# Kernel optimization log

Measured on AMD Instinct MI355X. Metric: run time of the kernel, lower is better.

The kernel has to match this reference:

```python
import jax, jax.numpy as jnp
import numpy as np

K = 7          # involution kernel size
PAD = 3        # (K-1)//2
G = 4          # groups = out_channels // group_channels
GC = 16        # group_channels
EPS = 1e-5     # BatchNorm eps


def _bn(x, g, b, m, v):
    # eval-mode BatchNorm2d over channel dim of NCHW
    scale = g / jnp.sqrt(v + EPS)
    return x * scale[:, None, None] + (b - m * scale)[:, None, None]


def _conv1x1(x, w, b=None):
    y = jnp.einsum('bchw,oc->bohw', x, w)
    if b is not None:
        y = y + b[:, None, None]
    return y


def _gelu(x):
    return jax.nn.gelu(x, approximate=False)  # torch nn.GELU default (erf)


def _involution(x, wr, gr, br, mr, vr, ws, bs):
    # kernel-generation branch: 1x1 reduce -> BN -> ReLU -> 1x1 span
    r = jax.nn.relu(_bn(_conv1x1(x, wr), gr, br, mr, vr))
    w = _conv1x1(r, ws, bs)                       # [B, G*K*K, H, W]
    B, _, H, W = w.shape
    w = w.reshape(B, G, K * K, H, W)
    # unfold x into KxK patches (channel-major then row-major kernel pos, matching nn.Unfold)
    xp = jnp.pad(x, ((0, 0), (0, 0), (PAD, PAD), (PAD, PAD)))
    patches = jnp.stack([xp[:, :, i:i + H, j:j + W]
                         for i in range(K) for j in range(K)], axis=2)  # [B, C, KK, H, W]
    patches = patches.reshape(B, G, GC, K * K, H, W)
    out = jnp.einsum('bgkhw,bgckhw->bgchw', w, patches)  # per-pixel dynamic kernel apply
    return out.reshape(B, G * GC, H, W)


def setup_inputs() -> dict:
    key = jax.random.key(0)
    ks = jax.random.split(key, 24)
    B, Cin, Cout, H, W = 4, 32, 64, 128, 128
    red = Cout // 4
    n = lambda k, s, sc: jax.random.normal(k, s, jnp.float32) * sc
    u = lambda k, s: jax.random.uniform(k, s, jnp.float32, 0.5, 1.5)
    inp = {
        'x': n(ks[0], (B, Cin, H, W), 1.0),
        'w1': n(ks[1], (Cout, Cin), 0.15),
        # involution: reduce conv + BN, span conv
        'wr': n(ks[2], (red, Cout), 0.12), 'gr': u(ks[3], (red,)), 'br': n(ks[4], (red,), 0.05),
        'mr': n(ks[5], (red,), 0.05), 'vr': u(ks[6], (red,)),
        'ws': n(ks[7], (K * K * G, red), 0.1), 'bs': n(ks[8], (K * K * G,), 0.02),
        # BN after involution
        'g1': u(ks[9], (Cout,)), 'b1': n(ks[10], (Cout,), 0.05),
        'm1': n(ks[11], (Cout,), 0.05), 'v1': u(ks[12], (Cout,)),
        # convblock2
        'w2': n(ks[13], (Cout, Cout), 0.12),
        'g2': u(ks[14], (Cout,)), 'b2': n(ks[15], (Cout,), 0.05),
        'm2': n(ks[16], (Cout,), 0.05), 'v2': u(ks[17], (Cout,)),
        # mapping (residual projection) conv has bias=True by default
        'wm': n(ks[18], (Cout, Cin), 0.15), 'bmap': n(ks[19], (Cout,), 0.02),
        'gm': u(ks[20], (Cout,)), 'betam': n(ks[21], (Cout,), 0.05),
        'mm': n(ks[22], (Cout,), 0.05), 'vm': u(ks[23], (Cout,)),
    }
    return inp


def reference(x, w1, wr, gr, br, mr, vr, ws, bs, g1, b1, m1, v1,
              w2, g2, b2, m2, v2, wm, bmap, gm, betam, mm, vm):
    x1 = _gelu(_conv1x1(x, w1))                                  # convblock
    x1 = _gelu(_bn(_involution(x1, wr, gr, br, mr, vr, ws, bs),
                   g1, b1, m1, v1))                              # involution + BN + GELU
    x1 = _bn(_conv1x1(x1, w2), g2, b2, m2, v2)                   # convblock2
    skip = _bn(_conv1x1(x, wm, bmap), gm, betam, mm, vm)         # mapping (Cin != Cout)
    return _gelu(x1 + skip)
```

## Files before the change

### kernel.cpp

```cpp
#include <hip/hip_runtime.h>
#include <hip/hip_bf16.h>
#include <math.h>

#define HW    16384
#define Bsz   4
#define CIN   32
#define COUT  64
#define RED   16
#define KKN   49
#define GG    4
#define PW    134
#define NHALO 25152
#define NZB   99
#define NPXB  1024

typedef __hip_bfloat16 bf16;
typedef __attribute__((ext_vector_type(8))) short bf16x8;
typedef __attribute__((ext_vector_type(4))) float f32x4;

__device__ __forceinline__ float gelu_f(float x) {
    return 0.5f * x * (1.0f + erff(x * 0.70710678118654752f));
}
__device__ __forceinline__ void unpack_bf2(unsigned u, float& lo, float& hi) {
    lo = __uint_as_float(u << 16);
    hi = __uint_as_float(u & 0xffff0000u);
}
__device__ __forceinline__ unsigned pack_bf2(float lo, float hi) {
    unsigned a = __float_as_uint(lo), b = __float_as_uint(hi);
    a += 0x7fff + ((a >> 16) & 1);
    b += 0x7fff + ((b >> 16) & 1);
    return (a >> 16) | (b & 0xffff0000u);
}
__device__ __forceinline__ unsigned short bf16r(float v) {
    unsigned a = __float_as_uint(v);
    a += 0x7fff + ((a >> 16) & 1);
    return (unsigned short)(a >> 16);
}

#define OFF_RBUF  9437184
#define OFF_PAR   22020096
#define OFF_XBF   22085632
#define PSHC_F 16
#define PSMV_F 80
#define PSC1_F 144
#define PSH1_F 208
#define BCAT 12288

__global__ __launch_bounds__(256, 4) void k1_all(
    const float* __restrict__ x, const float* __restrict__ w1,
    const float* __restrict__ wr, const float* __restrict__ gr,
    const float* __restrict__ br, const float* __restrict__ mr,
    const float* __restrict__ vr,
    const float* __restrict__ g1, const float* __restrict__ b1,
    const float* __restrict__ m1, const float* __restrict__ v1,
    const float* __restrict__ w2, const float* __restrict__ g2,
    const float* __restrict__ b2, const float* __restrict__ m2,
    const float* __restrict__ v2,
    const float* __restrict__ wm, const float* __restrict__ bmap,
    const float* __restrict__ gm, const float* __restrict__ betam,
    const float* __restrict__ mm, const float* __restrict__ vm,
    char* __restrict__ parb, unsigned* __restrict__ x1pad,
    unsigned short* __restrict__ xbf, float* __restrict__ rbuf)
{
    __shared__ float x1f[4][16][65];
    int bid = blockIdx.x, t = threadIdx.x;

    if (bid >= NPXB) {
        int hb = bid - NPXB;
        if (hb < NZB) {
            unsigned i = (unsigned)hb * 256u + (unsigned)t;
            if (i < NHALO) {
                unsigned plane = i / 1572u;
                unsigned rem = i - plane * 1572u;
                unsigned row, col;
                if (rem < 804u) {
                    unsigned rr = rem / 134u;
                    col = rem - rr * 134u;
                    row = rr < 3u ? rr : rr + 128u;
                } else {
                    unsigned r2 = rem - 804u;
                    unsigned rr = r2 / 6u;
                    unsigned cc = r2 - rr * 6u;
                    row = rr + 3u;
                    col = cc < 3u ? cc : cc + 128u;
                }
                uint4* q = (uint4*)x1pad + ((size_t)(plane * PW + row) * PW + col) * 2;
                q[0] = make_uint4(0u, 0u, 0u, 0u);
                q[1] = make_uint4(0u, 0u, 0u, 0u);
            }
        } else {
            float* parf = (float*)parb;
            unsigned short* wcat = (unsigned short*)(parb + BCAT);
            for (int i = t; i < 64 * 96; i += 256) {
                int o = i / 96, c = i - o * 96;
                float v;
                if (c < 64) {
                    float s2 = g2[o] * rsqrtf(v2[o] + 1e-5f);
                    float sm = gm[o] * rsqrtf(vm[o] + 1e-5f);
                    v = w2[o * COUT + c] * (s2 / sm);
                } else {
                    v = wm[o * CIN + (c - 64)];
                }
                wcat[i] = bf16r(v);
            }
            if (t < 64) {
                float s2 = g2[t] * rsqrtf(v2[t] + 1e-5f);
                float sm = gm[t] * rsqrtf(vm[t] + 1e-5f);
                parf[PSHC_F + t] = (b2[t] - m2[t] * s2) + (betam[t] + (bmap[t] - mm[t]) * sm);
                parf[PSMV_F + t] = sm;
                float s1 = g1[t] * rsqrtf(v1[t] + 1e-5f);
                parf[PSC1_F + t] = s1;
                parf[PSH1_F + t] = b1[t] - m1[t] * s1;
            }
        }
        return;
    }

    int lane = t & 63;
    int wave = t >> 6;
    int m15 = lane & 15, quad = lane >> 4;
    int base_gpx = bid * 64 + wave * 16;
    int b   = base_gpx >> 14;
    int px0 = base_gpx & (HW - 1);

    int gpx = base_gpx + m15;
    int p   = gpx & (HW - 1);
    unsigned apk[4];
#pragma unroll
    for (int d = 0; d < 4; ++d) {
        float lo = x[((size_t)(b * CIN + quad * 8 + 2 * d)) * HW + p];
        float hi = x[((size_t)(b * CIN + quad * 8 + 2 * d + 1)) * HW + p];
        apk[d] = pack_bf2(lo, hi);
    }
    union BU { uint4 q; bf16x8 v; };
    BU au; au.q = make_uint4(apk[0], apk[1], apk[2], apk[3]);
    bf16x8 Af = au.v;
    *(uint4*)&xbf[(size_t)gpx * 32 + quad * 8] = au.q;

    f32x4 acc[4];
#pragma unroll
    for (int nt = 0; nt < 4; ++nt) {
        int o = nt * 16 + m15;
        unsigned bpk[4];
#pragma unroll
        for (int d = 0; d < 4; ++d) {
            float lo = w1[o * CIN + quad * 8 + 2 * d];
            float hi = w1[o * CIN + quad * 8 + 2 * d + 1];
            bpk[d] = pack_bf2(lo, hi);
        }
        BU bu; bu.q = make_uint4(bpk[0], bpk[1], bpk[2], bpk[3]);
        f32x4 z = {0.f, 0.f, 0.f, 0.f};
        acc[nt] = __builtin_amdgcn_mfma_f32_16x16x32_bf16(Af, bu.v, z, 0, 0, 0);
    }
#pragma unroll
    for (int nt = 0; nt < 4; ++nt)
#pragma unroll
        for (int reg = 0; reg < 4; ++reg)
            x1f[wave][quad * 4 + reg][nt * 16 + m15] = gelu_f(acc[nt][reg]);

    __syncthreads();

    {
        int pxl = lane >> 2, g = lane & 3;
        int pp = px0 + pxl, h = pp >> 7, w = pp & 127;
        unsigned pk[8];
#pragma unroll
        for (int d = 0; d < 8; ++d)
            pk[d] = pack_bf2(x1f[wave][pxl][g * 16 + 2 * d],
                             x1f[wave][pxl][g * 16 + 2 * d + 1]);
        unsigned* xo = x1pad +
            ((size_t)((b * GG + g) * PW + (h + 3)) * PW + (w + 3)) * 8;
        *(uint4*)xo       = make_uint4(pk[0], pk[1], pk[2], pk[3]);
        *(uint4*)(xo + 4) = make_uint4(pk[4], pk[5], pk[6], pk[7]);
    }

    float sc  = gr[m15] * rsqrtf(vr[m15] + 1e-5f);
    float rsh = br[m15] - mr[m15] * sc;
    f32x4 racc = {0.f, 0.f, 0.f, 0.f};
#pragma unroll
    for (int kt = 0; kt < 2; ++kt) {
        bf16x8 A2, B2;
#pragma unroll
        for (int j = 0; j < 8; ++j) {
            A2[j] = (short)bf16r(x1f[wave][m15][kt * 32 + quad * 8 + j]);
            B2[j] = (short)bf16r(wr[m15 * 64 + kt * 32 + quad * 8 + j] * sc);
        }
        racc = __builtin_amdgcn_mfma_f32_16x16x32_bf16(A2, B2, racc, 0, 0, 0);
    }
#pragma unroll
    for (int reg = 0; reg < 4; ++reg) {
        int gp = base_gpx + quad * 4 + reg;
        rbuf[(size_t)gp * 16 + m15] = fmaxf(racc[reg] + rsh, 0.f);
    }
}

#define TAPC(kk, TA, TB)                                                  \
    {                                                                     \
        const float* wk = wrow + (kk) * RED;                              \
        float s = brow[(kk)];                                             \
        s += rA.x * wk[0];  s += rA.y * wk[1];                            \
        s += rA.z * wk[2];  s += rA.w * wk[3];                            \
        s += rB.x * wk[4];  s += rB.y * wk[5];                            \
        s += rB.z * wk[6];  s += rB.w * wk[7];                            \
        s += rC.x * wk[8];  s += rC.y * wk[9];                            \
        s += rC.z * wk[10]; s += rC.w * wk[11];                           \
        s += rD.x * wk[12]; s += rD.y * wk[13];                           \
        s += rD.z * wk[14]; s += rD.w * wk[15];                           \
        float lo, hi;                                                     \
        unpack_bf2((TA).x, lo, hi); acc[0] += s*lo; acc[1] += s*hi;       \
        unpack_bf2((TA).y, lo, hi); acc[2] += s*lo; acc[3] += s*hi;       \
        unpack_bf2((TA).z, lo, hi); acc[4] += s*lo; acc[5] += s*hi;       \
        unpack_bf2((TA).w, lo, hi); acc[6] += s*lo; acc[7] += s*hi;       \
        unpack_bf2((TB).x, lo, hi); acc[8] += s*lo; acc[9] += s*hi;       \
        unpack_bf2((TB).y, lo, hi); acc[10]+= s*lo; acc[11]+= s*hi;       \
        unpack_bf2((TB).z, lo, hi); acc[12]+= s*lo; acc[13]+= s*hi;       \
        unpack_bf2((TB).w, lo, hi); acc[14]+= s*lo; acc[15]+= s*hi;       \
    }

__global__ __launch_bounds__(256, 4) void k34_fused(
    const unsigned* __restrict__ x1pad, const float* __restrict__ rbuf,
    const float* __restrict__ wsp, const float* __restrict__ bsp,
    const char* __restrict__ parb, const unsigned short* __restrict__ xbf,
    float* __restrict__ out)
{
    __shared__ unsigned short x2t[64][88];

    const float* par = (const float*)parb;
    int t = threadIdx.x;
    int b = blockIdx.x >> 8;
    int pxblk = (blockIdx.x & 255) << 6;

    {
        int pxl = t & 63;
        int g = __builtin_amdgcn_readfirstlane(t >> 6);
        int p = pxblk + pxl;
        int h = p >> 7, w0 = p & 127;
        int bg = b * GG + g;

        const float4* rp = (const float4*)&rbuf[((size_t)b * HW + p) * 16];
        float4 rA = rp[0], rB = rp[1], rC = rp[2], rD = rp[3];

        const float* wrow = wsp + g * KKN * RED;
        const float* brow = bsp + g * KKN;
        const unsigned* tp = x1pad + ((size_t)(bg * PW + h) * PW + w0) * 8;

        float acc[RED];
#pragma unroll
        for (int c = 0; c < RED; ++c) acc[c] = 0.f;

        const unsigned* pn = tp + 8;
        uint4 cA0 = *(const uint4*)tp, cB0 = *(const uint4*)(tp + 4);
        uint4 cA1 = *(const uint4*)pn, cB1 = *(const uint4*)(pn + 4);
        int jj = 1;
#pragma unroll 1
        for (int k = 0; k < KKN - 1; k += 2) {
            const unsigned* q0 = pn + (jj == 6 ? (PW - 6) * 8 : 8);
            int j0 = (jj == 6) ? 0 : jj + 1;
            const unsigned* q1 = q0 + (j0 == 6 ? (PW - 6) * 8 : 8);
            jj = (j0 == 6) ? 0 : j0 + 1;
            uint4 nA0 = *(const uint4*)q0, nB0 = *(const uint4*)(q0 + 4);
            uint4 nA1 = *(const uint4*)q1, nB1 = *(const uint4*)(q1 + 4);
            TAPC(k,     cA0, cB0);
            TAPC(k + 1, cA1, cB1);
            pn = q1;
            cA0 = nA0; cB0 = nB0; cA1 = nA1; cB1 = nB1;
        }
        TAPC(KKN - 1, cA0, cB0);

        unsigned pk[8];
#pragma unroll
        for (int d = 0; d < 8; ++d) {
            int ch0 = g * RED + 2 * d, ch1 = ch0 + 1;
            float v0 = gelu_f(par[PSC1_F + ch0] * acc[2 * d]     + par[PSH1_F + ch0]);
            float v1 = gelu_f(par[PSC1_F + ch1] * acc[2 * d + 1] + par[PSH1_F + ch1]);
            pk[d] = pack_bf2(v0, v1);
        }
        unsigned* xo = (unsigned*)&x2t[pxl][g * RED];
        *(uint4*)xo       = make_uint4(pk[0], pk[1], pk[2], pk[3]);
        *(uint4*)(xo + 4) = make_uint4(pk[4], pk[5], pk[6], pk[7]);
    }

    __syncthreads();

    {
        int lane = t & 63, wave = t >> 6;
        int m15  = lane & 15;
        int quad = lane >> 4;
        int pxl0 = wave * 16;
        int px0  = pxblk + pxl0;

        const unsigned short* wcat = (const unsigned short*)(parb + BCAT);

        bf16x8 Bf[3][4];
#pragma unroll
        for (int kt = 0; kt < 3; ++kt)
#pragma unroll
            for (int nt = 0; nt < 4; ++nt)
                Bf[kt][nt] = *(const bf16x8*)&wcat[(nt * 16 + m15) * 96 + kt * 32 + quad * 8];

        bf16x8 Af[3];
        Af[0] = *(const bf16x8*)&x2t[pxl0 + m15][quad * 8];
        Af[1] = *(const bf16x8*)&x2t[pxl0 + m15][32 + quad * 8];
        Af[2] = *(const bf16x8*)&xbf[((size_t)(b * HW + px0 + m15)) * 32 + quad * 8];

        f32x4 acc[4];
#pragma unroll
        for (int nt = 0; nt < 4; ++nt) acc[nt] = (f32x4){0.f, 0.f, 0.f, 0.f};
#pragma unroll
        for (int kt = 0; kt < 3; ++kt)
#pragma unroll
            for (int nt = 0; nt < 4; ++nt)
                acc[nt] = __builtin_amdgcn_mfma_f32_16x16x32_bf16(
                    Af[kt], Bf[kt][nt], acc[nt], 0, 0, 0);

#pragma unroll
        for (int nt = 0; nt < 4; ++nt) {
            int o = nt * 16 + m15;
            float smv = par[PSMV_F + o], sh = par[PSHC_F + o];
            float* op = out + (size_t)(b * COUT + o) * HW + px0 + quad * 4;
#pragma unroll
            for (int reg = 0; reg < 4; ++reg)
                op[reg] = gelu_f(smv * acc[nt][reg] + sh);
        }
    }
}

extern "C" void kernel_launch(void* const* d_in, const int* in_sizes, int n_in,
                              void* d_out, int out_size, void* d_ws, size_t ws_size,
                              hipStream_t stream) {
    const float* x    = (const float*)d_in[0];
    const float* w1   = (const float*)d_in[1];
    const float* wr   = (const float*)d_in[2];
    const float* gr   = (const float*)d_in[3];
    const float* br   = (const float*)d_in[4];
    const float* mr   = (const float*)d_in[5];
    const float* vr   = (const float*)d_in[6];
    const float* wsp  = (const float*)d_in[7];
    const float* bsp  = (const float*)d_in[8];
    const float* g1   = (const float*)d_in[9];
    const float* b1   = (const float*)d_in[10];
    const float* m1   = (const float*)d_in[11];
    const float* v1   = (const float*)d_in[12];
    const float* w2   = (const float*)d_in[13];
    const float* g2   = (const float*)d_in[14];
    const float* b2   = (const float*)d_in[15];
    const float* m2   = (const float*)d_in[16];
    const float* v2   = (const float*)d_in[17];
    const float* wm   = (const float*)d_in[18];
    const float* bmap = (const float*)d_in[19];
    const float* gm   = (const float*)d_in[20];
    const float* betam= (const float*)d_in[21];
    const float* mm   = (const float*)d_in[22];
    const float* vm   = (const float*)d_in[23];

    unsigned*       x1pad = (unsigned*)d_ws;
    float*          rbuf  = (float*)((char*)d_ws + OFF_RBUF);
    char*           parb  = (char*)d_ws + OFF_PAR;
    unsigned short* xbf   = (unsigned short*)((char*)d_ws + OFF_XBF);

    k1_all<<<NPXB + NZB + 1, 256, 0, stream>>>(
        x, w1, wr, gr, br, mr, vr, g1, b1, m1, v1,
        w2, g2, b2, m2, v2, wm, bmap, gm, betam, mm, vm,
        parb, x1pad, xbf, rbuf);
    k34_fused<<<Bsz * GG * HW / 256, 256, 0, stream>>>(
        x1pad, rbuf, wsp, bsp, parb, xbf, (float*)d_out);
}
```

Before: 153.3 us.

## Stage involution halo rows in double-buffered shared memory for tap reuse

The involution tap loop previously read all 49 neighbourhood taps per pixel directly from global memory, so each input pixel was fetched up to 49 times by neighbouring threads. The block now cooperatively loads one padded 70-pixel row per group into a double-buffered LDS row buffer, prefetches the next row from global while computing the current row's 7 taps out of LDS, and synchronises once per row. This cuts redundant global/L2 traffic at the cost of about 18 KB of extra LDS per block, which may lower occupancy, plus seven block barriers.

```diff
diff --git a/kernel.cpp b/kernel.cpp
--- a/kernel.cpp
+++ b/kernel.cpp
@@ -13,6 +13,7 @@
 #define NHALO 25152
 #define NZB   99
 #define NPXB  1024
+#define ROWCHK 560
 
 typedef __hip_bfloat16 bf16;
 typedef __attribute__((ext_vector_type(8))) short bf16x8;
@@ -194,6 +195,10 @@
     }
 }
 
+#define LDTAP(J)                                                          \
+    uint4 A##J = rb[aidx + (J)];                                          \
+    uint4 B##J = rb[aidx + 70 + (J)];
+
 #define TAPC(kk, TA, TB)                                                  \
     {                                                                     \
         const float* wk = wrow + (kk) * RED;                              \
@@ -223,49 +228,83 @@
     const char* __restrict__ parb, const unsigned short* __restrict__ xbf,
     float* __restrict__ out)
 {
+    __shared__ uint4 rowbuf[2][ROWCHK];
     __shared__ unsigned short x2t[64][88];
 
     const float* par = (const float*)parb;
     int t = threadIdx.x;
     int b = blockIdx.x >> 8;
     int pxblk = (blockIdx.x & 255) << 6;
+    int bh = pxblk >> 7, bw = pxblk & 127;
+    int b4 = b * GG;
+
+    int c0 = t, c1 = t + 256, c2 = t + 512;
+    int has2 = (c2 < ROWCHK);
+    int g0 = c0 / 140, r0c = c0 - g0 * 140;
+    int hf0 = r0c / 70, px0c = r0c - hf0 * 70;
+    int g1c = c1 / 140, r1c = c1 - g1c * 140;
+    int hf1 = r1c / 70, px1c = r1c - hf1 * 70;
+    int g2c = has2 ? c2 / 140 : 3;
+    int r2c = (has2 ? c2 : ROWCHK - 1) - g2c * 140;
+    int hf2 = r2c / 70, px2c = r2c - hf2 * 70;
+    size_t off0 = ((size_t)((b4 + g0) * PW + bh) * PW + (bw + px0c)) * 8 + hf0 * 4;
+    size_t off1 = ((size_t)((b4 + g1c) * PW + bh) * PW + (bw + px1c)) * 8 + hf1 * 4;
+    size_t off2 = ((size_t)((b4 + g2c) * PW + bh) * PW + (bw + px2c)) * 8 + hf2 * 4;
 
     {
         int pxl = t & 63;
         int g = __builtin_amdgcn_readfirstlane(t >> 6);
-        int p = pxblk + pxl;
-        int h = p >> 7, w0 = p & 127;
-        int bg = b * GG + g;
-
-        const float4* rp = (const float4*)&rbuf[((size_t)b * HW + p) * 16];
+        int aidx = g * 140 + pxl;
+
+        const float4* rp = (const float4*)&rbuf[((size_t)b * HW + pxblk + pxl) * 16];
         float4 rA = rp[0], rB = rp[1], rC = rp[2], rD = rp[3];
 
         const float* wrow = wsp + g * KKN * RED;
         const float* brow = bsp + g * KKN;
-        const unsigned* tp = x1pad + ((size_t)(bg * PW + h) * PW + w0) * 8;
 
         float acc[RED];
 #pragma unroll
         for (int c = 0; c < RED; ++c) acc[c] = 0.f;
 
-        const unsigned* pn = tp + 8;
-        uint4 cA0 = *(const uint4*)tp, cB0 = *(const uint4*)(tp + 4);
-        uint4 cA1 = *(const uint4*)pn, cB1 = *(const uint4*)(pn + 4);
-        int jj = 1;
+        {
+            uint4 v0 = *(const uint4*)(x1pad + off0);
+            uint4 v1 = *(const uint4*)(x1pad + off1);
+            uint4 v2;
+            if (has2) v2 = *(const uint4*)(x1pad + off2);
+            rowbuf[0][c0] = v0;
+            rowbuf[0][c1] = v1;
+            if (has2) rowbuf[0][c2] = v2;
+        }
+        __syncthreads();
+
+        size_t roff = (size_t)PW * 8;
 #pragma unroll 1
-        for (int k = 0; k < KKN - 1; k += 2) {
-            const unsigned* q0 = pn + (jj == 6 ? (PW - 6) * 8 : 8);
-            int j0 = (jj == 6) ? 0 : jj + 1;
-            const unsigned* q1 = q0 + (j0 == 6 ? (PW - 6) * 8 : 8);
-            jj = (j0 == 6) ? 0 : j0 + 1;
-            uint4 nA0 = *(const uint4*)q0, nB0 = *(const uint4*)(q0 + 4);
-            uint4 nA1 = *(const uint4*)q1, nB1 = *(const uint4*)(q1 + 4);
-            TAPC(k,     cA0, cB0);
-            TAPC(k + 1, cA1, cB1);
-            pn = q1;
-            cA0 = nA0; cB0 = nB0; cA1 = nA1; cB1 = nB1;
-        }
-        TAPC(KKN - 1, cA0, cB0);
+        for (int i = 0; i < 7; ++i) {
+            uint4 w0v, w1v, w2v;
+            if (i < 6) {
+                size_t ro = (size_t)(i + 1) * roff;
+                w0v = *(const uint4*)(x1pad + off0 + ro);
+                w1v = *(const uint4*)(x1pad + off1 + ro);
+                if (has2) w2v = *(const uint4*)(x1pad + off2 + ro);
+            }
+
+            const uint4* rb = &rowbuf[i & 1][0];
+            LDTAP(0) LDTAP(1) LDTAP(2) LDTAP(3) LDTAP(4) LDTAP(5) LDTAP(6)
+            TAPC(i * 7 + 0, A0, B0)
+            TAPC(i * 7 + 1, A1, B1)
+            TAPC(i * 7 + 2, A2, B2)
+            TAPC(i * 7 + 3, A3, B3)
+            TAPC(i * 7 + 4, A4, B4)
+            TAPC(i * 7 + 5, A5, B5)
+            TAPC(i * 7 + 6, A6, B6)
+
+            if (i < 6) {
+                rowbuf[(i + 1) & 1][c0] = w0v;
+                rowbuf[(i + 1) & 1][c1] = w1v;
+                if (has2) rowbuf[(i + 1) & 1][c2] = w2v;
+            }
+            __syncthreads();
+        }
 
         unsigned pk[8];
 #pragma unroll
```

After: 218.6 us. +42.6%, slower.
